# Performance work log

Hardware: AMD Instinct MI355X
Metric: run time of the kernel (lower is better)

## Reference

```python
import jax, jax.numpy as jnp
import numpy as np
from jax import lax

N = 20000        # nodes
E = 320000       # directed edges (avg degree 16)
F_IN = 512       # input feature dim
HID = 64         # hidden_layer
K_NEI = 8        # sampled neighbors per node
L = K_NEI + 1    # local subgraph size (self + neighbors)
N_TPL = 10       # N_templates
NT = 8           # N_templates_nodes
N_CLS = 6
ALPHA = 0.5      # FGW trade-off
EPS = 0.1        # entropic regularization
N_OUTER = 3      # outer CG iterations
N_SINK = 5       # sinkhorn iterations per outer step


def setup_inputs() -> dict:
    rng = np.random.default_rng(0)
    src = rng.integers(0, N, E).astype(np.int64)
    dst = rng.integers(0, N, E).astype(np.int64)
    edge_index = np.stack([src, dst])

    # fixed-size neighbor table (pad with self, mask)
    nbr = np.full((N, K_NEI), -1, np.int64)
    cnt = np.zeros(N, np.int64)
    for s, d in zip(src, dst):
        c = cnt[s]
        if c < K_NEI:
            nbr[s, c] = d
            cnt[s] = c + 1
    pad = nbr < 0
    self_col = np.arange(N, dtype=np.int64)
    nbr = np.where(pad, self_col[:, None], nbr)
    nbr_mask = np.concatenate([np.ones((N, 1)), (~pad).astype(np.float64)], 1).astype(np.float32)

    # local adjacency among {self, neighbors}: [N, L, L]
    idx_full = np.concatenate([self_col[:, None], nbr], 1)  # [N, L]
    edge_keys = np.unique(src * N + dst)
    keys = idx_full[:, :, None] * N + idx_full[:, None, :]
    C_local = np.isin(keys, edge_keys).astype(np.float32)

    ks = jax.random.split(jax.random.key(0), 10)
    x = jax.random.normal(ks[0], (N, F_IN), jnp.float32)
    W1 = jax.random.normal(ks[1], (F_IN, HID), jnp.float32) / np.float32(np.sqrt(F_IN))
    b1 = jnp.zeros((HID,), jnp.float32)
    W2 = jax.random.normal(ks[2], (HID, HID), jnp.float32) / np.float32(np.sqrt(HID))
    b2 = jnp.zeros((HID,), jnp.float32)
    t = jax.random.uniform(ks[3], (N_TPL, NT, NT), jnp.float32)
    templates = 0.5 * (t + jnp.swapaxes(t, 1, 2))  # symmetric template adjacency
    templates_features = jax.random.normal(ks[4], (N_TPL, NT, HID), jnp.float32)
    Wlin = jax.random.normal(ks[5], (HID + N_TPL, N_CLS), jnp.float32) / np.float32(np.sqrt(HID + N_TPL))
    blin = jnp.zeros((N_CLS,), jnp.float32)
    return {"x": x, "edge_index": jnp.asarray(edge_index), "nbr_idx": jnp.asarray(nbr),
            "nbr_mask": jnp.asarray(nbr_mask), "C_local": jnp.asarray(C_local),
            "W1": W1, "b1": b1, "W2": W2, "b2": b2,
            "templates": templates, "templates_features": templates_features,
            "Wlin": Wlin, "blin": blin}


def gcn(x, W, b, src, dst, n):
    xw = x @ W
    sl = jnp.arange(n)
    s = jnp.concatenate([src, sl])
    d = jnp.concatenate([dst, sl])
    deg = jax.ops.segment_sum(jnp.ones_like(s, jnp.float32), d, num_segments=n)
    dinv = lax.rsqrt(deg)
    coef = dinv[s] * dinv[d]
    return jax.ops.segment_sum(xw[s] * coef[:, None], d, num_segments=n) + b


def fgw_dist(M, C1, h1, C2, h2):
    # entropic fused GW (square loss) with fixed iterations; padded rows have h1 = 0
    f1 = C1 * C1
    f2 = C2 * C2
    constC = (f1 @ h1)[:, None] + (f2 @ h2)[None, :]
    T0 = h1[:, None] * h2[None, :]

    def outer(T, _):
        tens = constC - 2.0 * (C1 @ T @ C2)
        G = (1.0 - ALPHA) * M + ALPHA * tens
        Kmat = jnp.exp(-G / EPS)

        def sink(carry, _):
            u, v = carry
            u = h1 / (Kmat @ v + 1e-16)
            v = h2 / (Kmat.T @ u + 1e-16)
            return (u, v), None

        (u, v), _ = lax.scan(sink, (jnp.ones_like(h1), jnp.ones_like(h2)), None, length=N_SINK)
        return u[:, None] * Kmat * v[None, :], None

    T, _ = lax.scan(outer, T0, None, length=N_OUTER)
    tens = constC - 2.0 * (C1 @ T @ C2)
    return jnp.sum(T * ((1.0 - ALPHA) * M + ALPHA * tens))


def distance_to_template(x, nbr_idx, nbr_mask, C_local, templates_features, templates):
    n = x.shape[0]
    idx_full = jnp.concatenate([jnp.arange(n)[:, None], nbr_idx], axis=1)  # [N, L]
    xl = x[idx_full]  # [N, L, HID]
    # squared euclidean cost to each template: [N, T, L, NT]
    inner = jnp.einsum('nld,tmd->ntlm', xl, templates_features)
    M = (jnp.sum(xl * xl, -1)[:, None, :, None]
         + jnp.sum(templates_features * templates_features, -1)[None, :, None, :]
         - 2.0 * inner)
    h1 = nbr_mask / jnp.sum(nbr_mask, -1, keepdims=True)  # [N, L]
    h2 = jnp.full((NT,), 1.0 / NT, jnp.float32)

    per_tpl = jax.vmap(fgw_dist, in_axes=(0, None, None, 0, None))
    per_node = jax.vmap(per_tpl, in_axes=(0, 0, 0, None, None))
    return per_node(M, C_local, h1, templates, h2)  # [N, N_TPL]


def reference(x, edge_index, nbr_idx, nbr_mask, C_local, W1, b1, W2, b2,
              templates, templates_features, Wlin, blin):
    src, dst = edge_index[0], edge_index[1]
    n = x.shape[0]
    h = jax.nn.relu(gcn(x, W1, b1, src, dst, n))
    h = gcn(h, W2, b2, src, dst, n)
    y = distance_to_template(h, nbr_idx, nbr_mask, C_local, templates_features, templates)
    out = jnp.concatenate([h, y], axis=1) @ Wlin + blin
    return jax.nn.relu(out)
```

## Files before the change

kernel.cpp:

```cpp
#include <hip/hip_runtime.h>


#define NN   20000
#define EE   320000
#define FIN  512
#define HID  64
#define KNEI 8
#define LSZ  9
#define NTPL 10
#define NTN  8
#define NCLS 6
#define CAP  48
#define GSLICE 4000

typedef unsigned short bf16_t;
typedef unsigned short us8 __attribute__((ext_vector_type(8)));

__device__ __forceinline__ float b2f(bf16_t u) {
  union { unsigned int i; float f; } v; v.i = ((unsigned int)u) << 16; return v.f;
}
__device__ __forceinline__ bf16_t f2b(float f) {
  union { float f; unsigned int i; } v; v.f = f;
  unsigned int x = v.i;
  return (bf16_t)((x + 0x7fffu + ((x >> 16) & 1u)) >> 16);
}
__device__ __forceinline__ float ldf(const void* p, long i, int fp32) {
  return fp32 ? ((const float*)p)[i] : b2f(((const bf16_t*)p)[i]);
}
__device__ __forceinline__ int ldi(const void* p, long i, int i64) {
  return i64 ? (int)((const long long*)p)[i] : ((const int*)p)[i];
}
__device__ __forceinline__ float frcp(float x) { return __builtin_amdgcn_rcpf(x); }

__global__ __launch_bounds__(256) void probe_kernel(const void* __restrict__ x,
                                                    const void* __restrict__ ei,
                                                    const void* __restrict__ tfeat,
                                                    int* __restrict__ flags,
                                                    float* __restrict__ tn2min,
                                                    int* __restrict__ pos) {
  int tid = threadIdx.x;
  int zi = blockIdx.x * 256 + tid;
  if (zi < NN) pos[zi] = 0;
  if (blockIdx.x != 0) return;

  __shared__ int sfl[2];
  __shared__ float tn2s[80];
  if (tid == 0) {
    int sane = 0;
    for (int k = 0; k < 64; k += 2) {
      bf16_t u = ((const bf16_t*)x)[k];
      int e = (u >> 7) & 0xff;
      if (e >= 112 && e <= 142) sane++;
    }
    int f0 = (sane < 24) ? 1 : 0;
    int zc = 0;
    for (int k = 1; k < 64; k += 2)
      if (((const int*)ei)[k] == 0) zc++;
    int f1 = (zc >= 16) ? 1 : 0;
    flags[0] = f0; flags[1] = f1;
    sfl[0] = f0; sfl[1] = f1;
  }
  __syncthreads();
  if (tid < 80) {
    int fF = sfl[0];
    float s = 0.f;
    for (int k = 0; k < HID; ++k) {
      float v = ldf(tfeat, (long)tid * HID + k, fF);
      s += v * v;
    }
    tn2s[tid] = s;
  }
  __syncthreads();
  if (tid == 0) {
    float gmin = 1e30f;
    for (int t = 0; t < NTPL; ++t) {
      float m = tn2s[t * 8];
      for (int r = 1; r < 8; ++r) m = fminf(m, tn2s[t * 8 + r]);
      tn2min[t] = m;
      gmin = fminf(gmin, m);
    }
    tn2min[NTPL] = gmin;
  }
}

__global__ __launch_bounds__(256) void scatter_kernel(const void* __restrict__ ei,
                                                      int* __restrict__ pos,
                                                      unsigned short* __restrict__ slot,
                                                      const int* __restrict__ flags) {
  int i = blockIdx.x * 256 + threadIdx.x;
  if (i >= EE) return;
  int i64 = flags[1];
  int s = ldi(ei, i, i64);
  int d = ldi(ei, (long)EE + i, i64);
  int p = atomicAdd(&pos[d], 1);
  if (p < CAP) slot[(long)d * CAP + p] = (unsigned short)s;
}

__global__ __launch_bounds__(256) void gemm1_kernel(const void* __restrict__ x,
                                                    const void* __restrict__ W1,
                                                    const int* __restrict__ cnt,
                                                    float* __restrict__ xw1,
                                                    const int* __restrict__ flags,
                                                    int rowbase) {
  int wave = blockIdx.x * 4 + (threadIdx.x >> 6);
  int lane = threadIdx.x & 63;
  int row0 = rowbase + wave * 4;
  if (row0 + 3 >= NN) {
    if (row0 >= NN) return;
  }
  float a0 = 0.f, a1 = 0.f, a2 = 0.f, a3 = 0.f;
  if (!flags[0]) {
    const bf16_t* xb = (const bf16_t*)x + (long)row0 * FIN;
    const bf16_t* wp = (const bf16_t*)W1;
#pragma unroll 2
    for (int k8 = 0; k8 < FIN / 8; ++k8) {
      us8 r0 = *(const us8*)(xb + k8 * 8);
      us8 r1 = *(const us8*)(xb + FIN + k8 * 8);
      us8 r2 = *(const us8*)(xb + 2 * FIN + k8 * 8);
      us8 r3 = *(const us8*)(xb + 3 * FIN + k8 * 8);
#pragma unroll
      for (int q = 0; q < 8; ++q) {
        float w = b2f(wp[(k8 * 8 + q) * HID + lane]);
        a0 += b2f(r0[q]) * w;
        a1 += b2f(r1[q]) * w;
        a2 += b2f(r2[q]) * w;
        a3 += b2f(r3[q]) * w;
      }
    }
  } else {
    const float* x0 = (const float*)x + (long)row0 * FIN;
    const float* wp = (const float*)W1;
#pragma unroll 8
    for (int k = 0; k < FIN; ++k) {
      float w = wp[k * HID + lane];
      a0 += x0[k] * w;
      a1 += x0[FIN + k] * w;
      a2 += x0[2 * FIN + k] * w;
      a3 += x0[3 * FIN + k] * w;
    }
  }
  float d0 = rsqrtf((float)cnt[row0 + 0] + 1.0f);
  float d1 = rsqrtf((float)cnt[row0 + 1] + 1.0f);
  float d2 = rsqrtf((float)cnt[row0 + 2] + 1.0f);
  float d3 = rsqrtf((float)cnt[row0 + 3] + 1.0f);
  xw1[(long)(row0 + 0) * HID + lane] = a0 * d0;
  xw1[(long)(row0 + 1) * HID + lane] = a1 * d1;
  xw1[(long)(row0 + 2) * HID + lane] = a2 * d2;
  xw1[(long)(row0 + 3) * HID + lane] = a3 * d3;
}

__global__ __launch_bounds__(256) void gatherA_kernel(const float* __restrict__ sxw,
                                                      const int* __restrict__ cnt,
                                                      const unsigned short* __restrict__ slot,
                                                      float* __restrict__ sxw2,
                                                      const void* __restrict__ b1v,
                                                      const void* __restrict__ W2,
                                                      const int* __restrict__ flags) {
  int n = blockIdx.x * 4 + (threadIdx.x >> 6);
  if (n >= NN) return;
  int fF = flags[0];
  int c = threadIdx.x & 63;
  float acc = sxw[(long)n * HID + c];
  int m = cnt[n]; if (m > CAP) m = CAP;
  const unsigned short* sl = slot + (long)n * CAP;
  float accB = 0.f;
  for (int e0 = 0; e0 < m; e0 += 8) {
    us8 s8 = *(const us8*)(sl + e0);
    if (e0 + 0 < m) acc  += sxw[(long)s8[0] * HID + c];
    if (e0 + 1 < m) accB += sxw[(long)s8[1] * HID + c];
    if (e0 + 2 < m) acc  += sxw[(long)s8[2] * HID + c];
    if (e0 + 3 < m) accB += sxw[(long)s8[3] * HID + c];
    if (e0 + 4 < m) acc  += sxw[(long)s8[4] * HID + c];
    if (e0 + 5 < m) accB += sxw[(long)s8[5] * HID + c];
    if (e0 + 6 < m) acc  += sxw[(long)s8[6] * HID + c];
    if (e0 + 7 < m) accB += sxw[(long)s8[7] * HID + c];
  }
  float dn = rsqrtf((float)cnt[n] + 1.0f);
  float h1 = (acc + accB) * dn + ldf(b1v, c, fF);
  h1 = h1 > 0.f ? h1 : 0.f;

  float o = 0.f;
#pragma unroll 8
  for (int k = 0; k < HID; ++k)
    o += __shfl(h1, k) * ldf(W2, k * HID + c, fF);
  sxw2[(long)n * HID + c] = o * dn;
}

__global__ __launch_bounds__(256) void gatherB_kernel(const float* __restrict__ sxw,
                                                      const int* __restrict__ cnt,
                                                      const unsigned short* __restrict__ slot,
                                                      float* __restrict__ h,
                                                      float* __restrict__ n2,
                                                      const void* __restrict__ b2v,
                                                      const int* __restrict__ flags) {
  int n = blockIdx.x * 4 + (threadIdx.x >> 6);
  if (n >= NN) return;
  int c = threadIdx.x & 63;
  float acc = sxw[(long)n * HID + c];
  int m = cnt[n]; if (m > CAP) m = CAP;
  const unsigned short* sl = slot + (long)n * CAP;
  float accB = 0.f;
  for (int e0 = 0; e0 < m; e0 += 8) {
    us8 s8 = *(const us8*)(sl + e0);
    if (e0 + 0 < m) acc  += sxw[(long)s8[0] * HID + c];
    if (e0 + 1 < m) accB += sxw[(long)s8[1] * HID + c];
    if (e0 + 2 < m) acc  += sxw[(long)s8[2] * HID + c];
    if (e0 + 3 < m) accB += sxw[(long)s8[3] * HID + c];
    if (e0 + 4 < m) acc  += sxw[(long)s8[4] * HID + c];
    if (e0 + 5 < m) accB += sxw[(long)s8[5] * HID + c];
    if (e0 + 6 < m) acc  += sxw[(long)s8[6] * HID + c];
    if (e0 + 7 < m) accB += sxw[(long)s8[7] * HID + c];
  }
  float dn = rsqrtf((float)cnt[n] + 1.0f);
  float h2 = (acc + accB) * dn;
  h[(long)n * HID + c] = h2;
  float v = h2 + ldf(b2v, c, flags[0]);
  float s = v * v;
  s += __shfl_xor(s, 1); s += __shfl_xor(s, 2); s += __shfl_xor(s, 4);
  s += __shfl_xor(s, 8); s += __shfl_xor(s, 16); s += __shfl_xor(s, 32);
  if (c == 0) n2[n] = s;
}

#define NODES_PB 4
#define TPN 80
#define XLP 65

__global__ __launch_bounds__(320, 2) void fgw_kernel(
    const float* __restrict__ h2,
    const void* __restrict__ b2v,
    const void* __restrict__ nbr_idx,
    const void* __restrict__ nbr_mask,
    const void* __restrict__ C_local,
    const void* __restrict__ tmpl,
    const void* __restrict__ tfeat,
    const void* __restrict__ Wlin,
    const void* __restrict__ blin,
    void* __restrict__ out,
    const int* __restrict__ flags,
    const float* __restrict__ tn2min,
    const float* __restrict__ n2)
{
  const int tid = threadIdx.x;
  const int fF = flags[0];
  const int fI = flags[1];
  const int nb = tid / TPN;
  const int local = tid - nb * TPN;
  const int t = local >> 3;
  const int j = local & 7;
  const int n = blockIdx.x * NODES_PB + nb;
  const int lane = tid & 63;
  const int ob = lane & 56;

  __shared__ float xlS[NODES_PB][LSZ][XLP];
  __shared__ float C1S[NODES_PB][81];
  __shared__ float hwS[NODES_PB][LSZ];
  __shared__ float f1S[NODES_PB][LSZ];
  __shared__ float xnS[NODES_PB][LSZ];
  __shared__ float distS[NODES_PB][NTPL];
  __shared__ float xmaxS[NODES_PB];
  __shared__ int   needS[NODES_PB];
  __shared__ int   sidxS[NODES_PB][LSZ];
  __shared__ float WlinS[(HID + NTPL) * NCLS + NCLS];

  for (int i = tid; i < (HID + NTPL) * NCLS; i += 320)
    WlinS[i] = ldf(Wlin, i, fF);
  if (tid < NCLS) WlinS[(HID + NTPL) * NCLS + tid] = ldf(blin, tid, fF);

  if (local < LSZ) {
    int idx = (local == 0) ? n : ldi(nbr_idx, (long)n * KNEI + local - 1, fI);
    sidxS[nb][local] = idx;
    xnS[nb][local] = n2[idx];
  }
  if (local < HID)
    xlS[nb][0][local] = h2[(long)n * HID + local] + ldf(b2v, local, fF);
  __syncthreads();

  if (local == 0) {
    float xm = xnS[nb][0];
#pragma unroll
    for (int l = 1; l < LSZ; ++l) xm = fmaxf(xm, xnS[nb][l]);
    xmaxS[nb] = xm;
    needS[nb] = ((sqrtf(tn2min[NTPL]) - sqrtf(xm)) >= 5.0990195f) ? 0 : 1;
  }
  __syncthreads();

  const int need = needS[nb];
  if (need) {
    for (int i = local; i < 8 * HID; i += TPN) {
      int l = 1 + (i >> 6), k = i & 63;
      xlS[nb][l][k] = h2[(long)sidxS[nb][l] * HID + k] + ldf(b2v, k, fF);
    }
    for (int i = local; i < 81; i += TPN)
      C1S[nb][i] = ldf(C_local, (long)n * 81 + i, fF);
  }
  __syncthreads();

  if (need && local < LSZ) {
    int l = local;
    float msum = 0.f, f1 = 0.f;
#pragma unroll
    for (int jj = 0; jj < LSZ; ++jj) {
      float mj = ldf(nbr_mask, (long)n * LSZ + jj, fF);
      msum += mj;
      float c = C1S[nb][l * LSZ + jj];
      f1 += c * c * mj;
    }
    float inv = frcp(msum);
    hwS[nb][l] = ldf(nbr_mask, (long)n * LSZ + l, fF) * inv;
    f1S[nb][l] = f1 * inv;
  }
  __syncthreads();

  bool slow = need && ((sqrtf(tn2min[t]) - sqrtf(xmaxS[nb])) < 5.0990195f);
  if (slow) {
    float C2c[NTN];
    float f2h2;
    {
      float s = 0.f;
#pragma unroll
      for (int m = 0; m < NTN; ++m) {
        C2c[m] = ldf(tmpl, t * 64 + m * 8 + j, fF);
        float r = ldf(tmpl, t * 64 + j * 8 + m, fF);
        s += r * r;
      }
      f2h2 = s * 0.125f;
    }
    float hwr[LSZ], f1r[LSZ];
#pragma unroll
    for (int l = 0; l < LSZ; ++l) { hwr[l] = hwS[nb][l]; f1r[l] = f1S[nb][l]; }

    float Mc[LSZ];
    {
      float accI[LSZ];
#pragma unroll
      for (int l = 0; l < LSZ; ++l) accI[l] = 0.f;
      float tn2 = 0.f;
      const long tb = (long)local * HID;
      for (int kb = 0; kb < 8; ++kb) {
        float r[8];
#pragma unroll
        for (int q = 0; q < 8; ++q) r[q] = ldf(tfeat, tb + kb * 8 + q, fF);
#pragma unroll
        for (int q = 0; q < 8; ++q) tn2 += r[q] * r[q];
#pragma unroll
        for (int l = 0; l < LSZ; ++l) {
          float s = 0.f;
#pragma unroll
          for (int q = 0; q < 8; ++q) s += xlS[nb][l][kb * 8 + q] * r[q];
          accI[l] += s;
        }
      }
#pragma unroll
      for (int l = 0; l < LSZ; ++l)
        Mc[l] = xnS[nb][l] + tn2 - 2.f * accI[l];
    }

    float Tc[LSZ], Kc[LSZ], u[LSZ];
#pragma unroll
    for (int l = 0; l < LSZ; ++l) Tc[l] = hwr[l] * 0.125f;

    float v = 1.0f;
    for (int outer = 0; outer < 3; ++outer) {
      float Ac[LSZ];
#pragma unroll
      for (int l = 0; l < LSZ; ++l) {
        float s = 0.f;
#pragma unroll
        for (int l2 = 0; l2 < LSZ; ++l2) s += C1S[nb][l * LSZ + l2] * Tc[l2];
        Ac[l] = s;
      }
#pragma unroll
      for (int l = 0; l < LSZ; ++l) {
        float s = 0.f;
#pragma unroll
        for (int m = 0; m < NTN; ++m) s += __shfl(Ac[l], ob + m) * C2c[m];
        float tens = f1r[l] + f2h2 - 2.f * s;
        Kc[l] = __expf(-5.0f * (Mc[l] + tens));
      }
      v = 1.0f;
      for (int it = 0; it < 5; ++it) {
#pragma unroll
        for (int l = 0; l < LSZ; ++l) {
          float p = Kc[l] * v;
          p += __shfl_xor(p, 1); p += __shfl_xor(p, 2); p += __shfl_xor(p, 4);
          u[l] = hwr[l] * frcp(p + 1e-16f);
        }
        float s = 0.f;
#pragma unroll
        for (int l = 0; l < LSZ; ++l) s += Kc[l] * u[l];
        v = 0.125f * frcp(s + 1e-16f);
      }
#pragma unroll
      for (int l = 0; l < LSZ; ++l) Tc[l] = u[l] * Kc[l] * v;
    }
    {
      float Ac[LSZ];
#pragma unroll
      for (int l = 0; l < LSZ; ++l) {
        float s = 0.f;
#pragma unroll
        for (int l2 = 0; l2 < LSZ; ++l2) s += C1S[nb][l * LSZ + l2] * Tc[l2];
        Ac[l] = s;
      }
      float cl = 0.f;
#pragma unroll
      for (int l = 0; l < LSZ; ++l) {
        float s = 0.f;
#pragma unroll
        for (int m = 0; m < NTN; ++m) s += __shfl(Ac[l], ob + m) * C2c[m];
        float tens = f1r[l] + f2h2 - 2.f * s;
        cl += Tc[l] * 0.5f * (Mc[l] + tens);
      }
      cl += __shfl_xor(cl, 1); cl += __shfl_xor(cl, 2); cl += __shfl_xor(cl, 4);
      if (j == 0) distS[nb][t] = cl;
    }
  } else if (j == 0) {
    distS[nb][t] = 0.f;
  }
  __syncthreads();

  if (local < NCLS) {
    int c = local;
    float acc = WlinS[(HID + NTPL) * NCLS + c];
#pragma unroll
    for (int k = 0; k < HID; ++k)
      acc += xlS[nb][0][k] * WlinS[k * NCLS + c];
#pragma unroll
    for (int tt = 0; tt < NTPL; ++tt)
      acc += distS[nb][tt] * WlinS[(HID + tt) * NCLS + c];
    float r = acc > 0.f ? acc : 0.f;
    if (fF) ((float*)out)[(long)n * NCLS + c] = r;
    else    ((bf16_t*)out)[(long)n * NCLS + c] = f2b(r);
  }
}

extern "C" void kernel_launch(void* const* d_in, const int* in_sizes, int n_in,
                              void* d_out, int out_size, void* d_ws, size_t ws_size,
                              hipStream_t stream) {
  (void)in_sizes; (void)n_in; (void)out_size; (void)ws_size;
  const void* x     = d_in[0];
  const void* ei    = d_in[1];
  const void* nbr   = d_in[2];
  const void* nmask = d_in[3];
  const void* Cl    = d_in[4];
  const void* W1    = d_in[5];
  const void* b1    = d_in[6];
  const void* W2    = d_in[7];
  const void* b2    = d_in[8];
  const void* tmpl  = d_in[9];
  const void* tfeat = d_in[10];
  const void* Wlin  = d_in[11];
  const void* blin  = d_in[12];

  int*            flags  = (int*)d_ws;
  float*          tn2min = (float*)d_ws + 4;
  float*          n2     = (float*)d_ws + 16;
  int*            pos    = (int*)(n2 + NN);
  unsigned short* slot   = (unsigned short*)(pos + NN);
  float*          bufA   = (float*)((int*)(pos + NN) + (long)CAP * NN / 2);
  float*          bufB   = bufA + (long)NN * HID;

  probe_kernel<<<79, 256, 0, stream>>>(x, ei, tfeat, flags, tn2min, pos);
  scatter_kernel<<<(EE + 255) / 256, 256, 0, stream>>>(ei, pos, slot, flags);

  for (int s = 0; s < 5; ++s)
    gemm1_kernel<<<GSLICE / 16, 256, 0, stream>>>(x, W1, pos, bufA, flags,
                                                  s * GSLICE);
  gatherA_kernel<<<NN / 4, 256, 0, stream>>>(bufA, pos, slot, bufB, b1, W2, flags);
  gatherB_kernel<<<NN / 4, 256, 0, stream>>>(bufB, pos, slot, bufA, n2, b2, flags);

  fgw_kernel<<<NN / NODES_PB, 320, 0, stream>>>(bufA, b2, nbr, nmask, Cl, tmpl,
                                                tfeat, Wlin, blin, d_out, flags,
                                                tn2min, n2);
}
```

Before: 328.9 us.

## Pad neighbor slots with a zero sentinel row and merge sliced GEMM launches

Pre-fills the neighbor slot table with a sentinel index that points to an extra zeroed row in each feature buffer, so the gather loops can drop their per-element bounds checks. The five sliced gemm1 launches are merged into a single launch, and template features in the FGW kernel are read as one vector load instead of eight scalar loads. The probe kernel now also has to write the whole slot table, which adds memory traffic. Gathers always process multiples of eight entries, so padding lanes do extra reads of the zero row.

```diff
diff --git a/kernel.cpp b/kernel.cpp
--- a/kernel.cpp
+++ b/kernel.cpp
@@ -11,7 +11,6 @@
 #define NTN  8
 #define NCLS 6
 #define CAP  48
-#define GSLICE 4000
 
 typedef unsigned short bf16_t;
 typedef unsigned short us8 __attribute__((ext_vector_type(8)));
@@ -37,10 +36,21 @@
                                                     const void* __restrict__ tfeat,
                                                     int* __restrict__ flags,
                                                     float* __restrict__ tn2min,
-                                                    int* __restrict__ pos) {
+                                                    int* __restrict__ pos,
+                                                    unsigned short* __restrict__ slot,
+                                                    float* __restrict__ bufA,
+                                                    float* __restrict__ bufB) {
   int tid = threadIdx.x;
-  int zi = blockIdx.x * 256 + tid;
-  if (zi < NN) pos[zi] = 0;
+  long gid = (long)blockIdx.x * 256 + tid;
+  if (gid < NN) pos[gid] = 0;
+  if (gid < (long)CAP * NN / 8) {
+    us8 v;
+#pragma unroll
+    for (int q = 0; q < 8; ++q) v[q] = (unsigned short)NN;
+    ((us8*)slot)[gid] = v;
+  }
+  if (blockIdx.x == 1 && tid < HID) bufA[(long)NN * HID + tid] = 0.f;
+  if (blockIdx.x == 2 && tid < HID) bufB[(long)NN * HID + tid] = 0.f;
   if (blockIdx.x != 0) return;
 
   __shared__ int sfl[2];
@@ -100,14 +110,11 @@
                                                     const void* __restrict__ W1,
                                                     const int* __restrict__ cnt,
                                                     float* __restrict__ xw1,
-                                                    const int* __restrict__ flags,
-                                                    int rowbase) {
+                                                    const int* __restrict__ flags) {
   int wave = blockIdx.x * 4 + (threadIdx.x >> 6);
   int lane = threadIdx.x & 63;
-  int row0 = rowbase + wave * 4;
-  if (row0 + 3 >= NN) {
-    if (row0 >= NN) return;
-  }
+  int row0 = wave * 4;
+  if (row0 >= NN) return;
   float a0 = 0.f, a1 = 0.f, a2 = 0.f, a3 = 0.f;
   if (!flags[0]) {
     const bf16_t* xb = (const bf16_t*)x + (long)row0 * FIN;
@@ -166,14 +173,14 @@
   float accB = 0.f;
   for (int e0 = 0; e0 < m; e0 += 8) {
     us8 s8 = *(const us8*)(sl + e0);
-    if (e0 + 0 < m) acc  += sxw[(long)s8[0] * HID + c];
-    if (e0 + 1 < m) accB += sxw[(long)s8[1] * HID + c];
-    if (e0 + 2 < m) acc  += sxw[(long)s8[2] * HID + c];
-    if (e0 + 3 < m) accB += sxw[(long)s8[3] * HID + c];
-    if (e0 + 4 < m) acc  += sxw[(long)s8[4] * HID + c];
-    if (e0 + 5 < m) accB += sxw[(long)s8[5] * HID + c];
-    if (e0 + 6 < m) acc  += sxw[(long)s8[6] * HID + c];
-    if (e0 + 7 < m) accB += sxw[(long)s8[7] * HID + c];
+    acc  += sxw[(long)s8[0] * HID + c];
+    accB += sxw[(long)s8[1] * HID + c];
+    acc  += sxw[(long)s8[2] * HID + c];
+    accB += sxw[(long)s8[3] * HID + c];
+    acc  += sxw[(long)s8[4] * HID + c];
+    accB += sxw[(long)s8[5] * HID + c];
+    acc  += sxw[(long)s8[6] * HID + c];
+    accB += sxw[(long)s8[7] * HID + c];
   }
   float dn = rsqrtf((float)cnt[n] + 1.0f);
   float h1 = (acc + accB) * dn + ldf(b1v, c, fF);
@@ -202,14 +209,14 @@
   float accB = 0.f;
   for (int e0 = 0; e0 < m; e0 += 8) {
     us8 s8 = *(const us8*)(sl + e0);
-    if (e0 + 0 < m) acc  += sxw[(long)s8[0] * HID + c];
-    if (e0 + 1 < m) accB += sxw[(long)s8[1] * HID + c];
-    if (e0 + 2 < m) acc  += sxw[(long)s8[2] * HID + c];
-    if (e0 + 3 < m) accB += sxw[(long)s8[3] * HID + c];
-    if (e0 + 4 < m) acc  += sxw[(long)s8[4] * HID + c];
-    if (e0 + 5 < m) accB += sxw[(long)s8[5] * HID + c];
-    if (e0 + 6 < m) acc  += sxw[(long)s8[6] * HID + c];
-    if (e0 + 7 < m) accB += sxw[(long)s8[7] * HID + c];
+    acc  += sxw[(long)s8[0] * HID + c];
+    accB += sxw[(long)s8[1] * HID + c];
+    acc  += sxw[(long)s8[2] * HID + c];
+    accB += sxw[(long)s8[3] * HID + c];
+    acc  += sxw[(long)s8[4] * HID + c];
+    accB += sxw[(long)s8[5] * HID + c];
+    acc  += sxw[(long)s8[6] * HID + c];
+    accB += sxw[(long)s8[7] * HID + c];
   }
   float dn = rsqrtf((float)cnt[n] + 1.0f);
   float h2 = (acc + accB) * dn;
@@ -338,8 +345,14 @@
       const long tb = (long)local * HID;
       for (int kb = 0; kb < 8; ++kb) {
         float r[8];
-#pragma unroll
-        for (int q = 0; q < 8; ++q) r[q] = ldf(tfeat, tb + kb * 8 + q, fF);
+        if (!fF) {
+          us8 v = *(const us8*)((const bf16_t*)tfeat + tb + kb * 8);
+#pragma unroll
+          for (int q = 0; q < 8; ++q) r[q] = b2f(v[q]);
+        } else {
+#pragma unroll
+          for (int q = 0; q < 8; ++q) r[q] = ((const float*)tfeat)[tb + kb * 8 + q];
+        }
 #pragma unroll
         for (int q = 0; q < 8; ++q) tn2 += r[q] * r[q];
 #pragma unroll
@@ -458,14 +471,13 @@
   int*            pos    = (int*)(n2 + NN);
   unsigned short* slot   = (unsigned short*)(pos + NN);
   float*          bufA   = (float*)((int*)(pos + NN) + (long)CAP * NN / 2);
-  float*          bufB   = bufA + (long)NN * HID;
-
-  probe_kernel<<<79, 256, 0, stream>>>(x, ei, tfeat, flags, tn2min, pos);
+  float*          bufB   = bufA + (long)(NN + 1) * HID;
+
+  probe_kernel<<<512, 256, 0, stream>>>(x, ei, tfeat, flags, tn2min, pos,
+                                        slot, bufA, bufB);
   scatter_kernel<<<(EE + 255) / 256, 256, 0, stream>>>(ei, pos, slot, flags);
 
-  for (int s = 0; s < 5; ++s)
-    gemm1_kernel<<<GSLICE / 16, 256, 0, stream>>>(x, W1, pos, bufA, flags,
-                                                  s * GSLICE);
+  gemm1_kernel<<<NN / 16, 256, 0, stream>>>(x, W1, pos, bufA, flags);
   gatherA_kernel<<<NN / 4, 256, 0, stream>>>(bufA, pos, slot, bufB, b1, W2, flags);
   gatherB_kernel<<<NN / 4, 256, 0, stream>>>(bufB, pos, slot, bufA, n2, b2, flags);
 
```

Result: faster. 302.2 us (median of 2 runs) (-8.1%).
